# Optimization experiments

Measured on AMD Instinct MI355X. Metric: run time of the kernel, lower is better.

The kernel has to match this reference:

```python
import jax, jax.numpy as jnp
import numpy as np

N_HEAD = 16


def setup_inputs() -> dict:
    key = jax.random.key(0)
    k1, k2, k3 = jax.random.split(key, 3)
    B, T, C = 2, 2048, 1024
    x = jax.random.normal(k1, (B, T, C), dtype=jnp.float32)
    Wqkv = jax.random.normal(k2, (C, 3 * C), dtype=jnp.float32) * 0.02
    bqkv = jnp.zeros((3 * C,), dtype=jnp.float32)
    Wproj = jax.random.normal(k3, (C, C), dtype=jnp.float32) * 0.02
    bproj = jnp.zeros((C,), dtype=jnp.float32)
    return {"x": x, "Wqkv": Wqkv, "bqkv": bqkv, "Wproj": Wproj, "bproj": bproj}


def reference(x, Wqkv, bqkv, Wproj, bproj):
    b, t, c = x.shape
    h = N_HEAD
    d = c // h  # head_dim
    # qkv projection, split into q,k,v per head: (b,t,3,h,d)
    qkv = (x @ Wqkv + bqkv).reshape(b, t, 3, h, d)
    q, k, v = qkv[:, :, 0], qkv[:, :, 1], qkv[:, :, 2]  # each (b,t,h,d)
    # Faithful quirk of original: n_state = head_dim // heads, scale = 1/sqrt(n_state)
    scale = jnp.float32(1.0 / np.sqrt(d // h))
    # attn_mode == 'all': dense non-causal attention
    w = jnp.einsum('bqhd,bkhd->bhqk', q, k)  # (b,h,t,t)
    w = jax.nn.softmax(w * scale, axis=-1)
    a = jnp.einsum('bhqk,bkhd->bqhd', w, v).reshape(b, t, c)
    return a @ Wproj + bproj
```

## Files before the change

### kernel.cpp

```cpp
#include <hip/hip_runtime.h>

typedef float floatx4 __attribute__((ext_vector_type(4)));
typedef float floatx16 __attribute__((ext_vector_type(16)));
typedef __bf16 bf16x8 __attribute__((ext_vector_type(8)));
typedef __bf16 bf16x4 __attribute__((ext_vector_type(4)));
typedef __bf16 bf16x2 __attribute__((ext_vector_type(2)));
typedef float floatx2 __attribute__((ext_vector_type(2)));

#define MFMA16 __builtin_amdgcn_mfma_f32_16x16x32_bf16
#define MFMA32 __builtin_amdgcn_mfma_f32_32x32x16_bf16

typedef const __attribute__((address_space(1))) void* gas_t;
typedef __attribute__((address_space(3))) void* las_t;
#define GLD16(g, l) __builtin_amdgcn_global_load_lds((gas_t)(g), (las_t)(l), 16, 0, 0)

static __device__ __forceinline__ unsigned short f2bf(float f) {
  union { float f; unsigned int u; } v; v.f = f;
  unsigned int r = v.u + 0x7fffu + ((v.u >> 16) & 1u);
  return (unsigned short)(r >> 16);
}

static __device__ __forceinline__ unsigned pk2(float a, float b) {
  floatx2 v; v[0] = a; v[1] = b;
  union { bf16x2 h; unsigned u; } u;
  u.h = __builtin_convertvector(v, bf16x2);
  return u.u;
}

static __device__ __forceinline__ void cast_transpose_tile(
    const float* __restrict__ in, unsigned short* __restrict__ out,
    int R, int C, int bx, int by) {
  const int r0 = by * 64, c0 = bx * 64;
  const int tid = threadIdx.x;
  __shared__ float tl[64][65];
  const int rr = tid >> 4, cc = (tid & 15) * 4;
#pragma unroll
  for (int i = 0; i < 4; ++i) {
    int row = rr + i * 16;
    float4 v = *(const float4*)(in + (size_t)(r0 + row) * C + c0 + cc);
    tl[row][cc] = v.x; tl[row][cc + 1] = v.y;
    tl[row][cc + 2] = v.z; tl[row][cc + 3] = v.w;
  }
  __syncthreads();
  const int cl = tid >> 2, rbase = (tid & 3) * 16;
  unsigned short o[16];
#pragma unroll
  for (int j = 0; j < 16; ++j) o[j] = f2bf(tl[rbase + j][cl]);
  unsigned short* dst = out + (size_t)(c0 + cl) * R + r0 + rbase;
  *(uint4*)dst = *(uint4*)o;
  *(uint4*)(dst + 8) = *(uint4*)(o + 8);
}

__global__ __launch_bounds__(256) void prologue_kernel(
    const float* __restrict__ x, unsigned short* __restrict__ Xb,
    const float* __restrict__ Wqkv, unsigned short* __restrict__ Wqkvt,
    const float* __restrict__ Wproj, unsigned short* __restrict__ Wprojt) {
  const int bid = blockIdx.x;
  if (bid < 4096) {
    int i = bid * 256 + threadIdx.x;
    float4 v = ((const float4*)x)[i];
    ushort4 o;
    o.x = f2bf(v.x); o.y = f2bf(v.y); o.z = f2bf(v.z); o.w = f2bf(v.w);
    ((ushort4*)Xb)[i] = o;
  } else if (bid < 4096 + 768) {
    int b2 = bid - 4096;
    cast_transpose_tile(Wqkv, Wqkvt, 1024, 3072, b2 % 48, b2 / 48);
  } else {
    int b3 = bid - 4096 - 768;
    cast_transpose_tile(Wproj, Wprojt, 1024, 1024, b3 % 16, b3 / 16);
  }
}

__global__ __launch_bounds__(256) void gemm_qkv(
    const unsigned short* __restrict__ A,
    const unsigned short* __restrict__ Bt,
    const float* __restrict__ bias,
    unsigned short* __restrict__ Q,
    unsigned short* __restrict__ Kc,
    unsigned short* __restrict__ Vt) {
  const int K = 1024;
  const int m0 = blockIdx.y * 128, n0 = blockIdx.x * 128;
  const int tid = threadIdx.x, w = tid >> 6, l = tid & 63;
  const int l16 = l & 15, lq = l >> 4;
  const int wm = w >> 1, wn = w & 1;
  const int which = n0 >> 10;

  __shared__ __align__(16) unsigned short SH[32768];

  floatx4 acc[4][4] = {};

  int sA[4], sB[4];
  unsigned ldso[4];
#pragma unroll
  for (int j = 0; j < 4; ++j) {
    int s = j * 256 + tid;
    int row = s >> 3, blk = (s & 7) ^ (row & 7);
    sA[j] = (m0 + row) * K + blk * 8;
    sB[j] = (n0 + row) * K + blk * 8;
    ldso[j] = (unsigned)(j * 256 + w * 64) * 8;
  }

#pragma unroll
  for (int j = 0; j < 4; ++j) {
    GLD16(A + sA[j], SH + ldso[j]);
    GLD16(Bt + sB[j], SH + 8192 + ldso[j]);
  }

  if (which == 2) {
    for (int k0 = 0; k0 < K; k0 += 64) {
      __syncthreads();
      const int cur = (k0 >> 6) & 1;
      if (k0 + 64 < K) {
        const int nxt = cur ^ 1;
#pragma unroll
        for (int j = 0; j < 4; ++j) {
          GLD16(A + sA[j] + k0 + 64, SH + nxt * 16384 + ldso[j]);
          GLD16(Bt + sB[j] + k0 + 64, SH + nxt * 16384 + 8192 + ldso[j]);
        }
      }
      const unsigned short* As = SH + cur * 16384;
      const unsigned short* Bs = SH + cur * 16384 + 8192;
#pragma unroll
      for (int kk = 0; kk < 2; ++kk) {
        bf16x8 af[4], bf[4];
#pragma unroll
        for (int mi = 0; mi < 4; ++mi) {
          int row = wm * 64 + mi * 16 + l16;
          int blk = (kk * 4 + lq) ^ (l16 & 7);
          af[mi] = *(const bf16x8*)(As + row * 64 + blk * 8);
        }
#pragma unroll
        for (int ni = 0; ni < 4; ++ni) {
          int row = wn * 64 + ni * 16 + l16;
          int blk = (kk * 4 + lq) ^ (l16 & 7);
          bf[ni] = *(const bf16x8*)(Bs + row * 64 + blk * 8);
        }
#pragma unroll
        for (int ni = 0; ni < 4; ++ni)
#pragma unroll
          for (int mi = 0; mi < 4; ++mi)
            acc[mi][ni] = MFMA16(af[mi], bf[ni], acc[mi][ni], 0, 0, 0);
      }
    }
    float bv[4];
#pragma unroll
    for (int ni = 0; ni < 4; ++ni) bv[ni] = bias[n0 + wn * 64 + ni * 16 + l16];
    __syncthreads();
    unsigned short* E = SH + w * 2304;
    const int bh = (m0 >> 11) * 16 + ((n0 & 1023) >> 6) + wn;
    const int tt0 = (m0 & 2047) + wm * 64;
    const int m8 = l & 7, bc = 16 * (m8 >> 1) + 4 * (m8 & 1);
#pragma unroll
    for (int p = 0; p < 2; ++p) {
#pragma unroll
      for (int n2 = 0; n2 < 2; ++n2) {
        int ni = p * 2 + n2;
#pragma unroll
        for (int mi = 0; mi < 4; ++mi) {
          floatx4 vv = acc[mi][ni] + bv[ni];
          *(bf16x4*)(E + (n2 * 16 + l16) * 72 + mi * 16 + lq * 4) =
              __builtin_convertvector(vv, bf16x4);
        }
      }
#pragma unroll
      for (int s = 0; s < 4; ++s) {
        int dl = s * 8 + (l >> 3);
        union { bf16x4 h[2]; bf16x8 v; } uu;
        uu.h[0] = *(const bf16x4*)(E + dl * 72 + bc);
        uu.h[1] = *(const bf16x4*)(E + dl * 72 + bc + 8);
        *(bf16x8*)(Vt + ((size_t)bh * 64 + p * 32 + dl) * 2048 + tt0 +
                   m8 * 8) = uu.v;
      }
    }
  } else {
    for (int k0 = 0; k0 < K; k0 += 64) {
      __syncthreads();
      const int cur = (k0 >> 6) & 1;
      if (k0 + 64 < K) {
        const int nxt = cur ^ 1;
#pragma unroll
        for (int j = 0; j < 4; ++j) {
          GLD16(A + sA[j] + k0 + 64, SH + nxt * 16384 + ldso[j]);
          GLD16(Bt + sB[j] + k0 + 64, SH + nxt * 16384 + 8192 + ldso[j]);
        }
      }
      const unsigned short* As = SH + cur * 16384;
      const unsigned short* Bs = SH + cur * 16384 + 8192;
#pragma unroll
      for (int kk = 0; kk < 2; ++kk) {
        bf16x8 af[4], bf[4];
#pragma unroll
        for (int mi = 0; mi < 4; ++mi) {
          int row = wm * 64 + mi * 16 + l16;
          int blk = (kk * 4 + lq) ^ (l16 & 7);
          af[mi] = *(const bf16x8*)(As + row * 64 + blk * 8);
        }
#pragma unroll
        for (int ni = 0; ni < 4; ++ni) {
          int row = wn * 64 + ni * 16 + l16;
          int blk = (kk * 4 + lq) ^ (l16 & 7);
          bf[ni] = *(const bf16x8*)(Bs + row * 64 + blk * 8);
        }
#pragma unroll
        for (int ni = 0; ni < 4; ++ni)
#pragma unroll
          for (int mi = 0; mi < 4; ++mi)
            acc[mi][ni] = MFMA16(bf[ni], af[mi], acc[mi][ni], 0, 0, 0);
      }
    }
    const float sc = (which == 0) ? 0.7213475204444817f : 1.0f;
    unsigned short* dst = (which == 0) ? Q : Kc;
    __syncthreads();
    unsigned short* E = SH + w * 2304;
    const int bh = (m0 >> 11) * 16 + ((n0 & 1023) >> 6) + wn;
    const size_t gbase = ((size_t)bh * 2048 + (m0 & 2047) + wm * 64) * 64;
#pragma unroll
    for (int p = 0; p < 2; ++p) {
#pragma unroll
      for (int m2 = 0; m2 < 2; ++m2) {
        int mi = p * 2 + m2;
#pragma unroll
        for (int ni = 0; ni < 4; ++ni) {
          int col0 = n0 + wn * 64 + ni * 16 + lq * 4;
          floatx4 bv = *(const floatx4*)(bias + col0);
          floatx4 vv = (acc[mi][ni] + bv) * sc;
          *(bf16x4*)(E + (m2 * 16 + l16) * 72 + ni * 16 + lq * 4) =
              __builtin_convertvector(vv, bf16x4);
        }
      }
#pragma unroll
      for (int s = 0; s < 4; ++s) {
        int rl = s * 8 + (l >> 3);
        bf16x8 vv = *(const bf16x8*)(E + rl * 72 + (l & 7) * 8);
        *(bf16x8*)(dst + gbase + (size_t)(p * 32 + rl) * 64 + (l & 7) * 8) =
            vv;
      }
    }
  }
}

__global__ __launch_bounds__(256, 2) void attn_kernel(
    const unsigned short* __restrict__ Q,
    const unsigned short* __restrict__ Kc,
    const unsigned short* __restrict__ Vt,
    unsigned short* __restrict__ AO) {
  const int T = 2048;
  const int bid = blockIdx.x;
  const int lin = (bid & 7) * 128 + (bid >> 3);
  const int bh = lin >> 5, q0 = (lin & 31) * 64;
  const int tid = threadIdx.x, w = tid >> 6, l = tid & 63;
  const int r31 = l & 31, g = l >> 5;
  const int kh = w >> 1, wq = w & 1;
  const int h128 = tid & 127;

  __shared__ __align__(16) unsigned short KVs[2][2][2][4096];

  bf16x8 qf[4];
  {
    const unsigned short* qr =
        Q + ((size_t)bh * T + q0 + wq * 32 + r31) * 64 + g * 8;
#pragma unroll
    for (int ds = 0; ds < 4; ++ds) qf[ds] = *(const bf16x8*)(qr + ds * 16);
  }

  floatx16 o_acc[2] = {};
  float l_lane = 0.f;

  const unsigned short* kbase = Kc + (size_t)bh * T * 64;
  const unsigned short* vbase = Vt + (size_t)bh * 64 * T;
  int kro[4], vro[4];
  unsigned ldso[4];
#pragma unroll
  for (int j = 0; j < 4; ++j) {
    int s = j * 128 + h128;
    int row = s >> 3, blk = (s & 7) ^ (row & 7);
    kro[j] = row * 64 + blk * 8;
    vro[j] = row * T + blk * 8;
    ldso[j] = (unsigned)(j * 128 + (h128 & 64)) * 8;
  }

  {
    const int c0 = kh * 16;
#pragma unroll
    for (int j = 0; j < 4; ++j) {
      GLD16(kbase + c0 * 4096 + kro[j], &KVs[0][kh][0][ldso[j]]);
      GLD16(vbase + c0 * 64 + vro[j], &KVs[1][kh][0][ldso[j]]);
    }
  }

  for (int it = 0; it < 16; ++it) {
    __syncthreads();
    if (it + 1 < 16) {
      const int cn = kh * 16 + it + 1, nb = (it + 1) & 1;
#pragma unroll
      for (int j = 0; j < 4; ++j) {
        GLD16(kbase + cn * 4096 + kro[j], &KVs[0][kh][nb][ldso[j]]);
        GLD16(vbase + cn * 64 + vro[j], &KVs[1][kh][nb][ldso[j]]);
      }
    }
    const unsigned short* kb = &KVs[0][kh][it & 1][0];
    const unsigned short* vb = &KVs[1][kh][it & 1][0];

    bf16x8 pf[4];
#pragma unroll
    for (int kt = 0; kt < 2; ++kt) {
      const int row = kt * 32 + r31, rx = row & 7;
      const unsigned short* kr = kb + row * 64;
      floatx16 z = {};
#pragma unroll
      for (int ds = 0; ds < 4; ++ds)
        z = MFMA32(*(const bf16x8*)(kr + ((ds * 2 + g) ^ rx) * 8), qf[ds], z,
                   0, 0, 0);

      float pe[16];
#pragma unroll
      for (int r = 0; r < 16; ++r) pe[r] = __builtin_amdgcn_exp2f(z[r]);
      l_lane += (((pe[0] + pe[1]) + (pe[2] + pe[3])) +
                 ((pe[4] + pe[5]) + (pe[6] + pe[7]))) +
                (((pe[8] + pe[9]) + (pe[10] + pe[11])) +
                 ((pe[12] + pe[13]) + (pe[14] + pe[15])));
#pragma unroll
      for (int s2 = 0; s2 < 2; ++s2) {
        union { unsigned u[4]; bf16x8 v; } pu;
        pu.u[0] = pk2(pe[8 * s2 + 0], pe[8 * s2 + 1]);
        pu.u[1] = pk2(pe[8 * s2 + 2], pe[8 * s2 + 3]);
        pu.u[2] = pk2(pe[8 * s2 + 4], pe[8 * s2 + 5]);
        pu.u[3] = pk2(pe[8 * s2 + 6], pe[8 * s2 + 7]);
        pf[kt * 2 + s2] = pu.v;
      }
    }

#pragma unroll
    for (int dt = 0; dt < 2; ++dt) {
      const int row = dt * 32 + r31, rx = row & 7;
      const unsigned short* vr = vb + row * 64;
#pragma unroll
      for (int s = 0; s < 4; ++s) {
        bf16x8 vf = *(const bf16x8*)(vr + ((s * 2 + g) ^ rx) * 8);
        o_acc[dt] = MFMA32(vf, pf[s], o_acc[dt], 0, 0, 0);
      }
    }
  }

  __syncthreads();
  float* oex = (float*)&KVs[0][0][0][0];
  float* Lex = oex + 128 * 36;
  if (kh == 1) {
    float* r = oex + (wq * 64 + l) * 36;
#pragma unroll
    for (int dt = 0; dt < 2; ++dt)
#pragma unroll
      for (int rq = 0; rq < 4; ++rq) {
        floatx4 ov;
        ov[0] = o_acc[dt][rq * 4 + 0]; ov[1] = o_acc[dt][rq * 4 + 1];
        ov[2] = o_acc[dt][rq * 4 + 2]; ov[3] = o_acc[dt][rq * 4 + 3];
        *(floatx4*)(r + dt * 16 + rq * 4) = ov;
      }
    Lex[wq * 64 + l] = l_lane;
  }
  __syncthreads();
  if (kh == 0) {
    const float* r = oex + (wq * 64 + l) * 36;
    float ls = l_lane + Lex[wq * 64 + l];
    ls += __shfl_xor(ls, 32, 64);
    float inv = 1.0f / ls;
    const int b = bh >> 4, h = bh & 15;
    const int t = q0 + wq * 32 + r31;
    unsigned short* ao = AO + ((size_t)b * 2048 + t) * 1024 + h * 64;
#pragma unroll
    for (int dt = 0; dt < 2; ++dt)
#pragma unroll
      for (int rq = 0; rq < 4; ++rq) {
        floatx4 ov;
        ov[0] = o_acc[dt][rq * 4 + 0]; ov[1] = o_acc[dt][rq * 4 + 1];
        ov[2] = o_acc[dt][rq * 4 + 2]; ov[3] = o_acc[dt][rq * 4 + 3];
        ov += *(const floatx4*)(r + dt * 16 + rq * 4);
        ov *= inv;
        *(bf16x4*)(ao + dt * 32 + rq * 8 + g * 4) =
            __builtin_convertvector(ov, bf16x4);
      }
  }
}

__global__ __launch_bounds__(256) void gemm_proj(
    const unsigned short* __restrict__ A,
    const unsigned short* __restrict__ Bt,
    const float* __restrict__ bias,
    float* __restrict__ out) {
  const int K = 1024, N = 1024;
  const int m0 = blockIdx.y * 128, n0 = blockIdx.x * 64;
  const int tid = threadIdx.x, w = tid >> 6, l = tid & 63;
  const int l16 = l & 15, lq = l >> 4;

  __shared__ __align__(16) unsigned short SH[24576];

  floatx4 acc[2][4] = {};

  int sA[4], sB[2];
  unsigned ldsoA[4], ldsoB[2];
#pragma unroll
  for (int j = 0; j < 4; ++j) {
    int s = j * 256 + tid;
    int row = s >> 3, blk = (s & 7) ^ (row & 7);
    sA[j] = (m0 + row) * K + blk * 8;
    ldsoA[j] = (unsigned)(j * 256 + w * 64) * 8;
  }
#pragma unroll
  for (int j = 0; j < 2; ++j) {
    int s = j * 256 + tid;
    int row = s >> 3, blk = (s & 7) ^ (row & 7);
    sB[j] = (n0 + row) * K + blk * 8;
    ldsoB[j] = (unsigned)(j * 256 + w * 64) * 8;
  }

#pragma unroll
  for (int j = 0; j < 4; ++j) GLD16(A + sA[j], SH + ldsoA[j]);
#pragma unroll
  for (int j = 0; j < 2; ++j) GLD16(Bt + sB[j], SH + 8192 + ldsoB[j]);

  for (int k0 = 0; k0 < K; k0 += 64) {
    __syncthreads();
    const int cur = (k0 >> 6) & 1;
    if (k0 + 64 < K) {
      const int nxt = cur ^ 1;
#pragma unroll
      for (int j = 0; j < 4; ++j)
        GLD16(A + sA[j] + k0 + 64, SH + nxt * 12288 + ldsoA[j]);
#pragma unroll
      for (int j = 0; j < 2; ++j)
        GLD16(Bt + sB[j] + k0 + 64, SH + nxt * 12288 + 8192 + ldsoB[j]);
    }
    const unsigned short* As = SH + cur * 12288;
    const unsigned short* Bs = SH + cur * 12288 + 8192;
#pragma unroll
    for (int kk = 0; kk < 2; ++kk) {
      bf16x8 af[2], bf[4];
#pragma unroll
      for (int mi = 0; mi < 2; ++mi) {
        int row = w * 32 + mi * 16 + l16;
        int blk = (kk * 4 + lq) ^ (l16 & 7);
        af[mi] = *(const bf16x8*)(As + row * 64 + blk * 8);
      }
#pragma unroll
      for (int ni = 0; ni < 4; ++ni) {
        int row = ni * 16 + l16;
        int blk = (kk * 4 + lq) ^ (l16 & 7);
        bf[ni] = *(const bf16x8*)(Bs + row * 64 + blk * 8);
      }
#pragma unroll
      for (int ni = 0; ni < 4; ++ni)
#pragma unroll
        for (int mi = 0; mi < 2; ++mi)
          acc[mi][ni] = MFMA16(bf[ni], af[mi], acc[mi][ni], 0, 0, 0);
    }
  }

#pragma unroll
  for (int mi = 0; mi < 2; ++mi) {
    int t = m0 + w * 32 + mi * 16 + l16;
#pragma unroll
    for (int ni = 0; ni < 4; ++ni) {
      int col0 = n0 + ni * 16 + lq * 4;
      floatx4 bv = *(const floatx4*)(bias + col0);
      *(floatx4*)(out + (size_t)t * N + col0) = acc[mi][ni] + bv;
    }
  }
}

extern "C" void kernel_launch(void* const* d_in, const int* in_sizes, int n_in,
                              void* d_out, int out_size, void* d_ws,
                              size_t ws_size, hipStream_t stream) {
  const float* x     = (const float*)d_in[0];
  const float* Wqkv  = (const float*)d_in[1];
  const float* bqkv  = (const float*)d_in[2];
  const float* Wproj = (const float*)d_in[3];
  const float* bproj = (const float*)d_in[4];
  float* out = (float*)d_out;

  unsigned short* Xb     = (unsigned short*)d_ws;
  unsigned short* Wqkvt  = Xb + 4194304;
  unsigned short* Wprojt = Wqkvt + 3145728;
  unsigned short* Qb     = Wprojt + 1048576;
  unsigned short* Kb     = Qb + 4194304;
  unsigned short* Vtb    = Kb + 4194304;
  unsigned short* AOb    = Vtb + 4194304;

  prologue_kernel<<<5120, 256, 0, stream>>>(x, Xb, Wqkv, Wqkvt, Wproj, Wprojt);
  gemm_qkv<<<dim3(24, 32), 256, 0, stream>>>(Xb, Wqkvt, bqkv, Qb, Kb, Vtb);
  attn_kernel<<<1024, 256, 0, stream>>>(Qb, Kb, Vtb, AOb);
  gemm_proj<<<dim3(16, 32), 256, 0, stream>>>(AOb, Wprojt, bproj, out);
}
```

Measured before the change: 173.7 us.

## Process 128 query rows per attention block to reuse K/V tiles across two query tiles

Each attention block now handles 128 query rows instead of 64: each wave holds two 32-row query tiles and reuses the K and V fragments it loads from shared memory for both. This halves the grid to 512 blocks and halves global K/V traffic per query. In exchange it doubles accumulator and Q-fragment registers, which may hurt occupancy at launch bounds of 2, and the larger end-of-kernel exchange buffer must still fit in the existing shared array.

```diff
diff --git a/kernel.cpp b/kernel.cpp
--- a/kernel.cpp
+++ b/kernel.cpp
@@ -246,8 +246,8 @@
     unsigned short* __restrict__ AO) {
   const int T = 2048;
   const int bid = blockIdx.x;
-  const int lin = (bid & 7) * 128 + (bid >> 3);
-  const int bh = lin >> 5, q0 = (lin & 31) * 64;
+  const int lin = (bid & 7) * 64 + (bid >> 3);
+  const int bh = lin >> 4, q0 = (lin & 15) * 128;
   const int tid = threadIdx.x, w = tid >> 6, l = tid & 63;
   const int r31 = l & 31, g = l >> 5;
   const int kh = w >> 1, wq = w & 1;
@@ -255,16 +255,17 @@
 
   __shared__ __align__(16) unsigned short KVs[2][2][2][4096];
 
-  bf16x8 qf[4];
-  {
+  bf16x8 qf[2][4];
+#pragma unroll
+  for (int qt = 0; qt < 2; ++qt) {
     const unsigned short* qr =
-        Q + ((size_t)bh * T + q0 + wq * 32 + r31) * 64 + g * 8;
-#pragma unroll
-    for (int ds = 0; ds < 4; ++ds) qf[ds] = *(const bf16x8*)(qr + ds * 16);
-  }
-
-  floatx16 o_acc[2] = {};
-  float l_lane = 0.f;
+        Q + ((size_t)bh * T + q0 + wq * 64 + qt * 32 + r31) * 64 + g * 8;
+#pragma unroll
+    for (int ds = 0; ds < 4; ++ds) qf[qt][ds] = *(const bf16x8*)(qr + ds * 16);
+  }
+
+  floatx16 o_acc[2][2] = {};
+  float l_lane[2] = {0.f, 0.f};
 
   const unsigned short* kbase = Kc + (size_t)bh * T * 64;
   const unsigned short* vbase = Vt + (size_t)bh * 64 * T;
@@ -301,32 +302,42 @@
     const unsigned short* kb = &KVs[0][kh][it & 1][0];
     const unsigned short* vb = &KVs[1][kh][it & 1][0];
 
-    bf16x8 pf[4];
+    bf16x8 kf[2][4];
 #pragma unroll
     for (int kt = 0; kt < 2; ++kt) {
       const int row = kt * 32 + r31, rx = row & 7;
       const unsigned short* kr = kb + row * 64;
-      floatx16 z = {};
 #pragma unroll
       for (int ds = 0; ds < 4; ++ds)
-        z = MFMA32(*(const bf16x8*)(kr + ((ds * 2 + g) ^ rx) * 8), qf[ds], z,
-                   0, 0, 0);
-
-      float pe[16];
-#pragma unroll
-      for (int r = 0; r < 16; ++r) pe[r] = __builtin_amdgcn_exp2f(z[r]);
-      l_lane += (((pe[0] + pe[1]) + (pe[2] + pe[3])) +
-                 ((pe[4] + pe[5]) + (pe[6] + pe[7]))) +
-                (((pe[8] + pe[9]) + (pe[10] + pe[11])) +
-                 ((pe[12] + pe[13]) + (pe[14] + pe[15])));
-#pragma unroll
-      for (int s2 = 0; s2 < 2; ++s2) {
-        union { unsigned u[4]; bf16x8 v; } pu;
-        pu.u[0] = pk2(pe[8 * s2 + 0], pe[8 * s2 + 1]);
-        pu.u[1] = pk2(pe[8 * s2 + 2], pe[8 * s2 + 3]);
-        pu.u[2] = pk2(pe[8 * s2 + 4], pe[8 * s2 + 5]);
-        pu.u[3] = pk2(pe[8 * s2 + 6], pe[8 * s2 + 7]);
-        pf[kt * 2 + s2] = pu.v;
+        kf[kt][ds] = *(const bf16x8*)(kr + ((ds * 2 + g) ^ rx) * 8);
+    }
+
+    bf16x8 pf[2][4];
+#pragma unroll
+    for (int qt = 0; qt < 2; ++qt) {
+#pragma unroll
+      for (int kt = 0; kt < 2; ++kt) {
+        floatx16 z = {};
+#pragma unroll
+        for (int ds = 0; ds < 4; ++ds)
+          z = MFMA32(kf[kt][ds], qf[qt][ds], z, 0, 0, 0);
+
+        float pe[16];
+#pragma unroll
+        for (int r = 0; r < 16; ++r) pe[r] = __builtin_amdgcn_exp2f(z[r]);
+        l_lane[qt] += (((pe[0] + pe[1]) + (pe[2] + pe[3])) +
+                       ((pe[4] + pe[5]) + (pe[6] + pe[7]))) +
+                      (((pe[8] + pe[9]) + (pe[10] + pe[11])) +
+                       ((pe[12] + pe[13]) + (pe[14] + pe[15])));
+#pragma unroll
+        for (int s2 = 0; s2 < 2; ++s2) {
+          union { unsigned u[4]; bf16x8 v; } pu;
+          pu.u[0] = pk2(pe[8 * s2 + 0], pe[8 * s2 + 1]);
+          pu.u[1] = pk2(pe[8 * s2 + 2], pe[8 * s2 + 3]);
+          pu.u[2] = pk2(pe[8 * s2 + 4], pe[8 * s2 + 5]);
+          pu.u[3] = pk2(pe[8 * s2 + 6], pe[8 * s2 + 7]);
+          pf[qt][kt * 2 + s2] = pu.v;
+        }
       }
     }
 
@@ -337,48 +348,60 @@
 #pragma unroll
       for (int s = 0; s < 4; ++s) {
         bf16x8 vf = *(const bf16x8*)(vr + ((s * 2 + g) ^ rx) * 8);
-        o_acc[dt] = MFMA32(vf, pf[s], o_acc[dt], 0, 0, 0);
+#pragma unroll
+        for (int qt = 0; qt < 2; ++qt)
+          o_acc[qt][dt] = MFMA32(vf, pf[qt][s], o_acc[qt][dt], 0, 0, 0);
       }
     }
   }
 
   __syncthreads();
   float* oex = (float*)&KVs[0][0][0][0];
-  float* Lex = oex + 128 * 36;
+  float* Lex = oex + 128 * 68;
   if (kh == 1) {
-    float* r = oex + (wq * 64 + l) * 36;
-#pragma unroll
-    for (int dt = 0; dt < 2; ++dt)
-#pragma unroll
-      for (int rq = 0; rq < 4; ++rq) {
-        floatx4 ov;
-        ov[0] = o_acc[dt][rq * 4 + 0]; ov[1] = o_acc[dt][rq * 4 + 1];
-        ov[2] = o_acc[dt][rq * 4 + 2]; ov[3] = o_acc[dt][rq * 4 + 3];
-        *(floatx4*)(r + dt * 16 + rq * 4) = ov;
-      }
-    Lex[wq * 64 + l] = l_lane;
+    float* r = oex + (wq * 64 + l) * 68;
+#pragma unroll
+    for (int qt = 0; qt < 2; ++qt) {
+#pragma unroll
+      for (int dt = 0; dt < 2; ++dt)
+#pragma unroll
+        for (int rq = 0; rq < 4; ++rq) {
+          floatx4 ov;
+          ov[0] = o_acc[qt][dt][rq * 4 + 0];
+          ov[1] = o_acc[qt][dt][rq * 4 + 1];
+          ov[2] = o_acc[qt][dt][rq * 4 + 2];
+          ov[3] = o_acc[qt][dt][rq * 4 + 3];
+          *(floatx4*)(r + qt * 32 + dt * 16 + rq * 4) = ov;
+        }
+      Lex[(wq * 64 + l) * 2 + qt] = l_lane[qt];
+    }
   }
   __syncthreads();
   if (kh == 0) {
-    const float* r = oex + (wq * 64 + l) * 36;
-    float ls = l_lane + Lex[wq * 64 + l];
-    ls += __shfl_xor(ls, 32, 64);
-    float inv = 1.0f / ls;
+    const float* r = oex + (wq * 64 + l) * 68;
     const int b = bh >> 4, h = bh & 15;
-    const int t = q0 + wq * 32 + r31;
-    unsigned short* ao = AO + ((size_t)b * 2048 + t) * 1024 + h * 64;
-#pragma unroll
-    for (int dt = 0; dt < 2; ++dt)
-#pragma unroll
-      for (int rq = 0; rq < 4; ++rq) {
-        floatx4 ov;
-        ov[0] = o_acc[dt][rq * 4 + 0]; ov[1] = o_acc[dt][rq * 4 + 1];
-        ov[2] = o_acc[dt][rq * 4 + 2]; ov[3] = o_acc[dt][rq * 4 + 3];
-        ov += *(const floatx4*)(r + dt * 16 + rq * 4);
-        ov *= inv;
-        *(bf16x4*)(ao + dt * 32 + rq * 8 + g * 4) =
-            __builtin_convertvector(ov, bf16x4);
-      }
+#pragma unroll
+    for (int qt = 0; qt < 2; ++qt) {
+      float ls = l_lane[qt] + Lex[(wq * 64 + l) * 2 + qt];
+      ls += __shfl_xor(ls, 32, 64);
+      float inv = 1.0f / ls;
+      const int t = q0 + wq * 64 + qt * 32 + r31;
+      unsigned short* ao = AO + ((size_t)b * 2048 + t) * 1024 + h * 64;
+#pragma unroll
+      for (int dt = 0; dt < 2; ++dt)
+#pragma unroll
+        for (int rq = 0; rq < 4; ++rq) {
+          floatx4 ov;
+          ov[0] = o_acc[qt][dt][rq * 4 + 0];
+          ov[1] = o_acc[qt][dt][rq * 4 + 1];
+          ov[2] = o_acc[qt][dt][rq * 4 + 2];
+          ov[3] = o_acc[qt][dt][rq * 4 + 3];
+          ov += *(const floatx4*)(r + qt * 32 + dt * 16 + rq * 4);
+          ov *= inv;
+          *(bf16x4*)(ao + dt * 32 + rq * 8 + g * 4) =
+              __builtin_convertvector(ov, bf16x4);
+        }
+    }
   }
 }
 
@@ -487,6 +510,6 @@
 
   prologue_kernel<<<5120, 256, 0, stream>>>(x, Xb, Wqkv, Wqkvt, Wproj, Wprojt);
   gemm_qkv<<<dim3(24, 32), 256, 0, stream>>>(Xb, Wqkvt, bqkv, Qb, Kb, Vtb);
-  attn_kernel<<<1024, 256, 0, stream>>>(Qb, Kb, Vtb, AOb);
+  attn_kernel<<<512, 256, 0, stream>>>(Qb, Kb, Vtb, AOb);
   gemm_proj<<<dim3(16, 32), 256, 0, stream>>>(AOb, Wprojt, bproj, out);
 }
```

Result: faster. 169.8 us (-2.3%).
